# Performance work log

Hardware: AMD Instinct MI355X
Metric: run time of the kernel (lower is better)

Reference implementation:

```python
import jax, jax.numpy as jnp
import numpy as np

NUM_NODES = 64
MAX_P = 8          # max parents per node (band width)
HID = 2 * MAX_P    # padded hidden size (per-node true hidden = 2*p)
BATCH = 131072


def _build_graph():
    """Banded lower-triangular DAG: node i>0 has parents max(0,i-8)..i-1; node 0 -> self."""
    A = np.zeros((NUM_NODES, NUM_NODES), np.int32)
    A[0, 0] = 1
    for i in range(1, NUM_NODES):
        A[i, max(0, i - MAX_P):i] = 1
    parent_idx = np.zeros((NUM_NODES, MAX_P), np.int32)
    in_mask = np.zeros((NUM_NODES, MAX_P), np.float32)
    for i in range(NUM_NODES):
        p = np.nonzero(A[i])[0]
        parent_idx[i, :len(p)] = p
        in_mask[i, :len(p)] = 1.0
    n_par = in_mask.sum(axis=1)  # (N,)
    # node i's true hidden width is 2*p_i; mask padded hidden units
    hid_mask = (np.arange(HID)[None, :] < 2 * n_par[:, None]).astype(np.float32)
    return parent_idx, in_mask, hid_mask


def setup_inputs() -> dict:
    key = jax.random.key(0)
    k_x, k_w1, k_b1, k_w2, k_b2 = jax.random.split(key, 5)
    parent_idx, in_mask, hid_mask = _build_graph()

    gt_labels = jax.random.normal(k_x, (BATCH, NUM_NODES), dtype=jnp.float32)

    # Padded per-node weights; zero out padded input columns / hidden rows so the
    # math equals the original ragged per-node Linear(p,2p)-Tanh-Linear(2p,1).
    bound1 = 1.0 / np.sqrt(MAX_P)
    W1 = jax.random.uniform(k_w1, (NUM_NODES, HID, MAX_P), jnp.float32, -bound1, bound1)
    b1 = jax.random.uniform(k_b1, (NUM_NODES, HID), jnp.float32, -bound1, bound1)
    bound2 = 1.0 / np.sqrt(HID)
    W2 = jax.random.uniform(k_w2, (NUM_NODES, HID), jnp.float32, -bound2, bound2)
    b2 = jax.random.uniform(k_b2, (NUM_NODES,), jnp.float32, -bound2, bound2)

    in_m = jnp.asarray(in_mask)       # (N, P)
    hid_m = jnp.asarray(hid_mask)     # (N, H)
    W1 = W1 * in_m[:, None, :] * hid_m[:, :, None]
    b1 = b1 * hid_m
    W2 = W2 * hid_m

    return {
        "gt_labels": gt_labels,
        "W1": W1, "b1": b1, "W2": W2, "b2": b2,
        "parent_idx": jnp.asarray(parent_idx),
    }


def reference(gt_labels, W1, b1, W2, b2, parent_idx):
    # Gather each node's (padded) parent values: (B, N, P)
    x = gt_labels[:, parent_idx]
    # Per-node tiny MLP, batched over nodes: hidden (B, N, H)
    h = jnp.tanh(jnp.einsum('bnp,nhp->bnh', x, W1) + b1)
    mus = (jnp.einsum('bnh,nh->bn', h, W2) + b2)[..., None]   # (B, N, 1)
    logvars = jnp.zeros_like(mus)
    return mus, logvars
```

## Files before the change

### kernel.cpp

```cpp
#include <hip/hip_runtime.h>


#define BATCH   131072
#define NODES   64
#define HID     16
#define MAXP    8
#define NBLOCKS 512
#define TPB     256
#define NWAVES  (NBLOCKS * (TPB / 64))
#define ROWS    (BATCH / NWAVES)

typedef float v2 __attribute__((ext_vector_type(2)));

__device__ __forceinline__ v2 tanh2(v2 x) {
    const v2 hi = {  3.5f,  3.5f };
    const v2 lo = { -3.5f, -3.5f };
    x = __builtin_elementwise_min(x, hi);
    x = __builtin_elementwise_max(x, lo);
    v2 x2  = x * x;
    v2 num = x2 * (x2 + 105.f) + 945.f;
    v2 den = x2 * (x2 * 15.f + 420.f) + 945.f;
    v2 r;
    r.x = __builtin_amdgcn_rcpf(den.x);
    r.y = __builtin_amdgcn_rcpf(den.y);
    return x * num * r;
}

__global__ __launch_bounds__(TPB, 2)
void prior_kernel(const float* __restrict__ gt,
                  const float* __restrict__ W1,
                  const float* __restrict__ b1,
                  const float* __restrict__ W2,
                  const float* __restrict__ b2,
                  const int*   __restrict__ parent_idx,
                  float* __restrict__ out)
{
    const int lane = threadIdx.x & 63;
    const int n    = lane;
    const int wave = blockIdx.x * (TPB / 64) + (threadIdx.x >> 6);

    v2 w1r[8][8];
    const float* w1p = W1 + n * (HID * MAXP);
    #pragma unroll
    for (int h2 = 0; h2 < 8; ++h2) {
        #pragma unroll
        for (int p = 0; p < 8; ++p) {
            v2 t = { w1p[(2 * h2) * MAXP + p], w1p[(2 * h2 + 1) * MAXP + p] };
            w1r[h2][p] = t;
        }
    }
    v2 b1r[8], w2r[8];
    #pragma unroll
    for (int h2 = 0; h2 < 8; ++h2) {
        v2 tb = { b1[n * HID + 2 * h2], b1[n * HID + 2 * h2 + 1] };
        v2 tw = { W2[n * HID + 2 * h2], W2[n * HID + 2 * h2 + 1] };
        b1r[h2] = tb;
        w2r[h2] = tw;
    }
    const float b2s = b2[n];
    int pidx[8];
    #pragma unroll
    for (int p = 0; p < 8; ++p) pidx[p] = parent_idx[n * MAXP + p];

    int   b     = wave;
    float g     = gt[b * NODES + n];
    float gnext = 0.f;
    for (int r = 0; r < ROWS; ++r) {
        const int bn = b + NWAVES;
        if (r + 1 < ROWS) gnext = gt[bn * NODES + n];

        float x[8];
        #pragma unroll
        for (int p = 0; p < 8; ++p) x[p] = __shfl(g, pidx[p], 64);

        v2 mu2 = { 0.f, 0.f };
        #pragma unroll
        for (int h2 = 0; h2 < 8; ++h2) {
            v2 a = b1r[h2];
            #pragma unroll
            for (int p = 0; p < 8; ++p) {
                v2 xb = { x[p], x[p] };
                a = __builtin_elementwise_fma(xb, w1r[h2][p], a);
            }
            v2 t = tanh2(a);
            mu2 = __builtin_elementwise_fma(t, w2r[h2], mu2);
        }
        const float mu = mu2.x + mu2.y + b2s;

        out[b * NODES + n] = mu;
        out[BATCH * NODES + b * NODES + n] = 0.f;

        g = gnext;
        b = bn;
    }
}

extern "C" void kernel_launch(void* const* d_in, const int* in_sizes, int n_in,
                              void* d_out, int out_size, void* d_ws, size_t ws_size,
                              hipStream_t stream)
{
    const float* gt  = (const float*)d_in[0];
    const float* W1  = (const float*)d_in[1];
    const float* b1  = (const float*)d_in[2];
    const float* W2  = (const float*)d_in[3];
    const float* b2  = (const float*)d_in[4];
    const int*   pix = (const int*)d_in[5];
    float* out = (float*)d_out;

    prior_kernel<<<NBLOCKS, TPB, 0, stream>>>(gt, W1, b1, W2, b2, pix, out);
}
```

Baseline: 147.9 us.

## Split nodes and hidden units across wave pairs to raise occupancy

Each batch row is now handled by a pair of waves, each covering 32 nodes. Within a wave, the two half-waves split the 16 hidden units, and the two partial sums are combined with a cross-half shuffle. This halves the per-thread weight registers, which allows launch bounds of 4 with twice as many blocks. The upper half-wave writes the zero logvar output while the lower writes mu. The parent gather becomes a contiguous ds_bpermute, and the tanh input clamp is removed; without it the rational approximation is wrong for large pre-activations, which is a correctness risk.

```diff
diff --git a/kernel.cpp b/kernel.cpp
--- a/kernel.cpp
+++ b/kernel.cpp
@@ -5,18 +5,15 @@
 #define NODES   64
 #define HID     16
 #define MAXP    8
-#define NBLOCKS 512
 #define TPB     256
-#define NWAVES  (NBLOCKS * (TPB / 64))
-#define ROWS    (BATCH / NWAVES)
+#define NBLOCKS 1024
+#define WVB     (TPB / 64)
+#define NPAIRS  (NBLOCKS * WVB / 2)
+#define ROWS    (BATCH / NPAIRS)
 
 typedef float v2 __attribute__((ext_vector_type(2)));
 
 __device__ __forceinline__ v2 tanh2(v2 x) {
-    const v2 hi = {  3.5f,  3.5f };
-    const v2 lo = { -3.5f, -3.5f };
-    x = __builtin_elementwise_min(x, hi);
-    x = __builtin_elementwise_max(x, lo);
     v2 x2  = x * x;
     v2 num = x2 * (x2 + 105.f) + 945.f;
     v2 den = x2 * (x2 * 15.f + 420.f) + 945.f;
@@ -26,7 +23,7 @@
     return x * num * r;
 }
 
-__global__ __launch_bounds__(TPB, 2)
+__global__ __launch_bounds__(TPB, 4)
 void prior_kernel(const float* __restrict__ gt,
                   const float* __restrict__ W1,
                   const float* __restrict__ b1,
@@ -36,62 +33,74 @@
                   float* __restrict__ out)
 {
     const int lane = threadIdx.x & 63;
-    const int n    = lane;
-    const int wave = blockIdx.x * (TPB / 64) + (threadIdx.x >> 6);
+    const int wv   = blockIdx.x * WVB + (threadIdx.x >> 6);
+    const int pair = wv >> 1;
+    const int hb   = wv & 1;
+    const int base = hb << 5;
+    const int sn   = lane & 31;
+    const int n    = base + sn;
+    const int hh   = lane >> 5;
 
-    v2 w1r[8][8];
-    const float* w1p = W1 + n * (HID * MAXP);
-    #pragma unroll
-    for (int h2 = 0; h2 < 8; ++h2) {
+    v2 w1r[4][8];
+    v2 b1r[4], w2r[4];
+    {
+        const float* w1p = W1 + (n * HID + hh * 8) * MAXP;
         #pragma unroll
-        for (int p = 0; p < 8; ++p) {
-            v2 t = { w1p[(2 * h2) * MAXP + p], w1p[(2 * h2 + 1) * MAXP + p] };
-            w1r[h2][p] = t;
+        for (int h2 = 0; h2 < 4; ++h2)
+            #pragma unroll
+            for (int p = 0; p < 8; ++p) {
+                v2 t = { w1p[(2 * h2) * MAXP + p], w1p[(2 * h2 + 1) * MAXP + p] };
+                w1r[h2][p] = t;
+            }
+        const float* b1p = b1 + n * HID + hh * 8;
+        const float* w2p = W2 + n * HID + hh * 8;
+        #pragma unroll
+        for (int h2 = 0; h2 < 4; ++h2) {
+            v2 tb = { b1p[2 * h2], b1p[2 * h2 + 1] };
+            v2 tw = { w2p[2 * h2], w2p[2 * h2 + 1] };
+            b1r[h2] = tb;
+            w2r[h2] = tw;
         }
     }
-    v2 b1r[8], w2r[8];
-    #pragma unroll
-    for (int h2 = 0; h2 < 8; ++h2) {
-        v2 tb = { b1[n * HID + 2 * h2], b1[n * HID + 2 * h2 + 1] };
-        v2 tw = { W2[n * HID + 2 * h2], W2[n * HID + 2 * h2 + 1] };
-        b1r[h2] = tb;
-        w2r[h2] = tw;
-    }
     const float b2s = b2[n];
-    int pidx[8];
-    #pragma unroll
-    for (int p = 0; p < 8; ++p) pidx[p] = parent_idx[n * MAXP + p];
 
-    int   b     = wave;
-    float g     = gt[b * NODES + n];
-    float gnext = 0.f;
+    int src = base - 8 + lane;
+    src = src < 0 ? 0 : (src > 63 ? 63 : src);
+    const int jb4 = (parent_idx[n * MAXP] - (base - 8)) << 2;
+
+    const long STR = (long)NPAIRS * NODES;
+    const float* gp = gt + (long)pair * NODES + src;
+    float*       op = out + (long)pair * NODES + base + sn
+                          + (hh ? (long)BATCH * NODES : 0);
+
+    float g = *gp;
     for (int r = 0; r < ROWS; ++r) {
-        const int bn = b + NWAVES;
-        if (r + 1 < ROWS) gnext = gt[bn * NODES + n];
+        gp += STR;
+        float gn = (r + 1 < ROWS) ? *gp : 0.f;
 
+        const int gi = __float_as_int(g);
         float x[8];
         #pragma unroll
-        for (int p = 0; p < 8; ++p) x[p] = __shfl(g, pidx[p], 64);
+        for (int p = 0; p < 8; ++p)
+            x[p] = __int_as_float(__builtin_amdgcn_ds_bpermute(jb4 + (p << 2), gi));
 
         v2 mu2 = { 0.f, 0.f };
         #pragma unroll
-        for (int h2 = 0; h2 < 8; ++h2) {
+        for (int h2 = 0; h2 < 4; ++h2) {
             v2 a = b1r[h2];
             #pragma unroll
             for (int p = 0; p < 8; ++p) {
                 v2 xb = { x[p], x[p] };
                 a = __builtin_elementwise_fma(xb, w1r[h2][p], a);
             }
-            v2 t = tanh2(a);
-            mu2 = __builtin_elementwise_fma(t, w2r[h2], mu2);
+            mu2 = __builtin_elementwise_fma(tanh2(a), w2r[h2], mu2);
         }
-        const float mu = mu2.x + mu2.y + b2s;
+        float s  = mu2.x + mu2.y;
+        float mu = s + __shfl_xor(s, 32, 64) + b2s;
 
-        out[b * NODES + n] = mu;
-        out[BATCH * NODES + b * NODES + n] = 0.f;
-
-        g = gnext;
-        b = bn;
+        *op = hh ? 0.f : mu;
+        op += STR;
+        g = gn;
     }
 }
 
```

After: 155.6 us. 5.2% more time.

## Compute per-node MLP hidden layer with fp16 MFMA over node pairs

Applied to the files above, without the earlier changes.

Replaces the per-lane scalar FMA evaluation of each node's 16x8 first layer with a 32x32x16 f16 MFMA. Each wave handles two nodes, and the batch rows form the N dimension. Parent values are loaded as contiguous 8-float vectors from the first parent index, which relies on the banded contiguous-parent graph. The grid is reorganized to 2048 blocks with occupancy hint 4, and the tanh clamp is removed. This is meant to remove the VALU bottleneck, but it adds fp16 rounding of inputs and weights, and an unclamped rational tanh that diverges for large pre-activations.

```diff
diff --git a/kernel.cpp b/kernel.cpp
--- a/kernel.cpp
+++ b/kernel.cpp
@@ -5,18 +5,18 @@
 #define NODES   64
 #define HID     16
 #define MAXP    8
-#define NBLOCKS 512
 #define TPB     256
-#define NWAVES  (NBLOCKS * (TPB / 64))
-#define ROWS    (BATCH / NWAVES)
+#define NBLOCKS 2048
+#define TM      32
+#define UNITS   16
 
-typedef float v2 __attribute__((ext_vector_type(2)));
+typedef float v2     __attribute__((ext_vector_type(2)));
+typedef float v4     __attribute__((ext_vector_type(4)));
+typedef float f32x16 __attribute__((ext_vector_type(16)));
+typedef _Float16 h8v __attribute__((ext_vector_type(8)));
+typedef unsigned u32x4 __attribute__((ext_vector_type(4)));
 
 __device__ __forceinline__ v2 tanh2(v2 x) {
-    const v2 hi = {  3.5f,  3.5f };
-    const v2 lo = { -3.5f, -3.5f };
-    x = __builtin_elementwise_min(x, hi);
-    x = __builtin_elementwise_max(x, lo);
     v2 x2  = x * x;
     v2 num = x2 * (x2 + 105.f) + 945.f;
     v2 den = x2 * (x2 * 15.f + 420.f) + 945.f;
@@ -26,7 +26,11 @@
     return x * num * r;
 }
 
-__global__ __launch_bounds__(TPB, 2)
+__device__ __forceinline__ unsigned pk16(float a, float b) {
+    return __builtin_bit_cast(unsigned, __builtin_amdgcn_cvt_pkrtz(a, b));
+}
+
+__global__ __launch_bounds__(TPB, 4)
 void prior_kernel(const float* __restrict__ gt,
                   const float* __restrict__ W1,
                   const float* __restrict__ b1,
@@ -36,62 +40,81 @@
                   float* __restrict__ out)
 {
     const int lane = threadIdx.x & 63;
-    const int n    = lane;
-    const int wave = blockIdx.x * (TPB / 64) + (threadIdx.x >> 6);
+    const int widx = threadIdx.x >> 6;
+    const int q    = blockIdx.x >> 8;
+    const int tc   = blockIdx.x & 255;
+    const int pair = q * 4 + widx;
+    const int n0   = pair * 2, n1 = n0 + 1;
+    const int sl   = lane & 31;
+    const int half = lane >> 5;
 
-    v2 w1r[8][8];
-    const float* w1p = W1 + n * (HID * MAXP);
+    h8v afrag;
     #pragma unroll
-    for (int h2 = 0; h2 < 8; ++h2) {
+    for (int j = 0; j < 8; ++j) {
+        float w = 0.f;
+        if (!half) { if (sl < 16)  w = W1[(n0 * HID + sl) * MAXP + j]; }
+        else       { if (sl >= 16) w = W1[(n1 * HID + (sl - 16)) * MAXP + j]; }
+        afrag[j] = (_Float16)w;
+    }
+
+    f32x16 cfrag;
+    float  w2f[16];
+    #pragma unroll
+    for (int r = 0; r < 16; ++r) {
+        const int m = (r & 3) + 8 * (r >> 2) + 4 * half;
+        cfrag[r] = (m < 16) ? b1[n0 * HID + m] : b1[n1 * HID + (m - 16)];
+        w2f[r]   = (m < 16) ? W2[n0 * HID + m] : W2[n1 * HID + (m - 16)];
+    }
+    v2 w2v[8];
+    #pragma unroll
+    for (int i = 0; i < 8; ++i) { v2 t = { w2f[2 * i], w2f[2 * i + 1] }; w2v[i] = t; }
+    const float b2v0 = b2[n0], b2v1 = b2[n1];
+
+    const int nd = half ? n1 : n0;
+    const int cs = parent_idx[nd * MAXP];
+    const unsigned rbase   = (unsigned)tc * 512u + (unsigned)sl;
+    unsigned       idx     = rbase * 64u + (unsigned)cs;
+    const unsigned ISTEP   = (unsigned)TM * 64u;
+    const unsigned idxLast = idx + (UNITS - 1) * ISTEP;
+    unsigned       om      = rbase * 64u + (unsigned)nd;
+    const unsigned LV      = (unsigned)BATCH * 64u;
+
+    v4 r0 = *(const v4*)(gt + idx);
+    v4 r1 = *(const v4*)(gt + idx + 4);
+
+    #pragma unroll 1
+    for (int t = 0; t < UNITS; ++t) {
+        unsigned nidx = idx + ISTEP;
+        if (nidx > idxLast) nidx = idxLast;
+        v4 rn0 = *(const v4*)(gt + nidx);
+        v4 rn1 = *(const v4*)(gt + nidx + 4);
+        idx = nidx;
+
+        u32x4 upk = { pk16(r0.x, r0.y), pk16(r0.z, r0.w),
+                      pk16(r1.x, r1.y), pk16(r1.z, r1.w) };
+        h8v bfrag = __builtin_bit_cast(h8v, upk);
+
+        f32x16 acc = __builtin_amdgcn_mfma_f32_32x32x16_f16(afrag, bfrag, cfrag, 0, 0, 0);
+
+        v2 s0 = { 0.f, 0.f }, s1 = { 0.f, 0.f };
         #pragma unroll
-        for (int p = 0; p < 8; ++p) {
-            v2 t = { w1p[(2 * h2) * MAXP + p], w1p[(2 * h2 + 1) * MAXP + p] };
-            w1r[h2][p] = t;
+        for (int i = 0; i < 4; ++i) {
+            v2 a = { acc[2 * i], acc[2 * i + 1] };
+            s0 = __builtin_elementwise_fma(tanh2(a), w2v[i], s0);
         }
-    }
-    v2 b1r[8], w2r[8];
-    #pragma unroll
-    for (int h2 = 0; h2 < 8; ++h2) {
-        v2 tb = { b1[n * HID + 2 * h2], b1[n * HID + 2 * h2 + 1] };
-        v2 tw = { W2[n * HID + 2 * h2], W2[n * HID + 2 * h2 + 1] };
-        b1r[h2] = tb;
-        w2r[h2] = tw;
-    }
-    const float b2s = b2[n];
-    int pidx[8];
-    #pragma unroll
-    for (int p = 0; p < 8; ++p) pidx[p] = parent_idx[n * MAXP + p];
+        #pragma unroll
+        for (int i = 4; i < 8; ++i) {
+            v2 a = { acc[2 * i], acc[2 * i + 1] };
+            s1 = __builtin_elementwise_fma(tanh2(a), w2v[i], s1);
+        }
+        float S0 = s0.x + s0.y;  S0 += __shfl_xor(S0, 32, 64);
+        float S1 = s1.x + s1.y;  S1 += __shfl_xor(S1, 32, 64);
+        const float mu = half ? (S1 + b2v1) : (S0 + b2v0);
 
-    int   b     = wave;
-    float g     = gt[b * NODES + n];
-    float gnext = 0.f;
-    for (int r = 0; r < ROWS; ++r) {
-        const int bn = b + NWAVES;
-        if (r + 1 < ROWS) gnext = gt[bn * NODES + n];
-
-        float x[8];
-        #pragma unroll
-        for (int p = 0; p < 8; ++p) x[p] = __shfl(g, pidx[p], 64);
-
-        v2 mu2 = { 0.f, 0.f };
-        #pragma unroll
-        for (int h2 = 0; h2 < 8; ++h2) {
-            v2 a = b1r[h2];
-            #pragma unroll
-            for (int p = 0; p < 8; ++p) {
-                v2 xb = { x[p], x[p] };
-                a = __builtin_elementwise_fma(xb, w1r[h2][p], a);
-            }
-            v2 t = tanh2(a);
-            mu2 = __builtin_elementwise_fma(t, w2r[h2], mu2);
-        }
-        const float mu = mu2.x + mu2.y + b2s;
-
-        out[b * NODES + n] = mu;
-        out[BATCH * NODES + b * NODES + n] = 0.f;
-
-        g = gnext;
-        b = bn;
+        out[om]      = mu;
+        out[om + LV] = 0.f;
+        om += ISTEP;
+        r0 = rn0; r1 = rn1;
     }
 }
 
```

Measured after the change: 170.8 us. 1.15x slower.
